# Performance work log

Hardware: AMD Instinct MI355X
Metric: run time of the kernel (lower is better)

## Reference

```python
import jax, jax.numpy as jnp
import numpy as np

BN_EPS = 1e-3  # O-CNN default bn_eps


def setup_inputs() -> dict:
    key = jax.random.key(0)
    k1, k2, k3 = jax.random.split(key, 3)
    N, Cin, Cout, K = 100000, 32, 32, 27  # nodes, channels, 3x3x3 taps
    data_in = jax.random.normal(k1, (1, Cin, N, 1), dtype=jnp.float32)
    neigh = jax.random.randint(k2, (N, K), 0, N, dtype=jnp.int32)
    weight = jax.random.normal(k3, (K, Cin, Cout), dtype=jnp.float32) * 0.05
    gamma = jnp.ones((Cout,), dtype=jnp.float32)
    beta = jnp.zeros((Cout,), dtype=jnp.float32)
    return {"data_in": data_in, "neigh": neigh, "weight": weight,
            "gamma": gamma, "beta": beta}


def reference(data_in, neigh, weight, gamma, beta):
    # data_in: [1, Cin, N, 1] -> x: [N, Cin]
    x = data_in[0, :, :, 0].T
    # Octree conv: gather 27 neighbor features per node, then small matmul.
    col = x[neigh]                                   # [N, 27, Cin] (irregular gather)
    y = jnp.einsum('nkc,kcd->nd', col, weight)       # [N, Cout]
    # BatchNorm2d in training mode: stats over the N (spatial) axis.
    mean = jnp.mean(y, axis=0)
    var = jnp.mean(jnp.square(y - mean), axis=0)     # biased variance, as BN uses
    yn = (y - mean) * jax.lax.rsqrt(var + BN_EPS) * gamma + beta
    # back to O-CNN layout [1, Cout, N, 1]
    return yn.T[None, :, :, None]
```

## Files before the change

### kernel.cpp

```cpp
#include <hip/hip_runtime.h>

#define KK 27

typedef short bf16x8 __attribute__((ext_vector_type(8)));
typedef float f32x4  __attribute__((ext_vector_type(4)));

__device__ inline unsigned short f2bf(float f) {
    unsigned u = __float_as_uint(f);
    unsigned r = u + 0x7fffu + ((u >> 16) & 1u);
    return (unsigned short)(r >> 16);
}

__global__ __launch_bounds__(256) void prep_k(const float* __restrict__ in,
                                              const float* __restrict__ w,
                                              unsigned short* __restrict__ xTb,
                                              unsigned short* __restrict__ wTb,
                                              float* __restrict__ tot,
                                              int N, int nxblk) {
    __shared__ float tile[32][33];
    const int b = blockIdx.x;
    if (b < nxblk) {
        int n0 = b * 32;
        int tx = threadIdx.x & 31;
        int ty = threadIdx.x >> 5;
#pragma unroll
        for (int c = ty; c < 32; c += 8) {
            int n = n0 + tx;
            tile[c][tx] = (n < N) ? in[(long)c * N + n] : 0.f;
        }
        __syncthreads();
#pragma unroll
        for (int nn = ty; nn < 32; nn += 8) {
            int n = n0 + nn;
            if (n < N) xTb[(long)n * 32 + tx] = f2bf(tile[tx][nn]);
        }
        if (b == 0 && threadIdx.x < 32) xTb[(long)N * 32 + threadIdx.x] = 0;
    } else {
        int k = b - nxblk;
        for (int i = threadIdx.x; i < 1024; i += 256) {
            int cin = i >> 5, cout = i & 31;
            wTb[k * 1024 + cout * 32 + cin] = f2bf(w[k * 1024 + cin * 32 + cout]);
        }
        if (k == 0) {
            for (int i = threadIdx.x; i < 32 * 64; i += 256) tot[i] = 0.f;
        }
    }
}

__global__ __launch_bounds__(64, 4) void conv_k(const unsigned short* __restrict__ xTb,
                                                const int* __restrict__ neigh,
                                                const unsigned short* __restrict__ wTb,
                                                float* __restrict__ y,
                                                float* __restrict__ tot,
                                                int N) {
    __shared__ float ct[16][33];

    const int L    = threadIdx.x;
    const int r16  = L & 15;
    const int quad = L >> 4;
    const int base = blockIdx.x * 16;
    const int n0   = base + r16;
    const bool v0  = (n0 < N);
    const long nb0 = (long)(v0 ? n0 : 0) * KK;

    f32x4 acc0 = {0.f, 0.f, 0.f, 0.f};
    f32x4 acc1 = acc0;

    bf16x8 A[3], B0[3], B1[3];
    int ja[3];

#pragma unroll
    for (int d = 0; d < 3; ++d) ja[d] = v0 ? neigh[nb0 + d] : N;
#pragma unroll
    for (int d = 0; d < 3; ++d) {
        A[d]  = *(const bf16x8*)(xTb + (long)ja[d] * 32 + quad * 8);
        const unsigned short* wn = wTb + d * 1024;
        B0[d] = *(const bf16x8*)(wn + r16 * 32 + quad * 8);
        B1[d] = *(const bf16x8*)(wn + (16 + r16) * 32 + quad * 8);
        ja[d] = v0 ? neigh[nb0 + d + 3] : N;
    }

#pragma unroll
    for (int t = 0; t < KK; ++t) {
        const int cur = t % 3;
        acc0 = __builtin_amdgcn_mfma_f32_16x16x32_bf16(A[cur], B0[cur], acc0, 0, 0, 0);
        acc1 = __builtin_amdgcn_mfma_f32_16x16x32_bf16(A[cur], B1[cur], acc1, 0, 0, 0);
        if (t + 3 < KK) {
            A[cur]  = *(const bf16x8*)(xTb + (long)ja[cur] * 32 + quad * 8);
            const unsigned short* wn = wTb + (t + 3) * 1024;
            B0[cur] = *(const bf16x8*)(wn + r16 * 32 + quad * 8);
            B1[cur] = *(const bf16x8*)(wn + (16 + r16) * 32 + quad * 8);
            if (t + 6 < KK) ja[cur] = v0 ? neigh[nb0 + t + 6] : N;
        }
    }

    float s0 = 0.f, q0 = 0.f, s1 = 0.f, q1 = 0.f;
#pragma unroll
    for (int r = 0; r < 4; ++r) {
        s0 += acc0[r];
        q0 += acc0[r] * acc0[r];
        s1 += acc1[r];
        q1 += acc1[r] * acc1[r];
    }
#pragma unroll
    for (int off = 16; off < 64; off <<= 1) {
        s0 += __shfl_xor(s0, off, 64);
        q0 += __shfl_xor(q0, off, 64);
        s1 += __shfl_xor(s1, off, 64);
        q1 += __shfl_xor(q1, off, 64);
    }
    const int stripe = blockIdx.x & 31;
    if (L < 16) {
        float* tb = tot + stripe * 64;
        atomicAdd(&tb[L],      s0);
        atomicAdd(&tb[L + 16], s1);
        atomicAdd(&tb[L + 32], q0);
        atomicAdd(&tb[L + 48], q1);
    }

#pragma unroll
    for (int r = 0; r < 4; ++r) {
        ct[quad * 4 + r][r16]      = acc0[r];
        ct[quad * 4 + r][16 + r16] = acc1[r];
    }
    __syncthreads();
    const int node = L & 15;
    const int ch   = L >> 4;
    const int gn   = base + node;
    if (gn < N) {
#pragma unroll
        for (int i = 0; i < 8; ++i) {
            const int cout = ch * 8 + i;
            y[(long)cout * N + gn] = ct[node][cout];
        }
    }
}

__global__ __launch_bounds__(256) void norm_k(float* __restrict__ y,
                                              const float* __restrict__ tot,
                                              const float* __restrict__ gamma,
                                              const float* __restrict__ beta, int N) {
    const int d = blockIdx.y;
    float sm = 0.f, sq = 0.f;
#pragma unroll
    for (int s = 0; s < 32; ++s) {
        sm += tot[s * 64 + d];
        sq += tot[s * 64 + 32 + d];
    }
    const float mean = sm / (float)N;
    const float var  = sq / (float)N - mean * mean;
    const float sc   = gamma[d] * rsqrtf(var + 1e-3f);
    const float sh   = beta[d] - mean * sc;

    int i = blockIdx.x * blockDim.x + threadIdx.x;
    int base = i * 4;
    if (base + 3 < N) {
        float4* p = (float4*)(y + (long)d * N + base);
        float4 v = *p;
        v.x = fmaf(v.x, sc, sh);
        v.y = fmaf(v.y, sc, sh);
        v.z = fmaf(v.z, sc, sh);
        v.w = fmaf(v.w, sc, sh);
        *p = v;
    } else if (base < N) {
        for (int t = base; t < N; ++t) y[(long)d * N + t] = fmaf(y[(long)d * N + t], sc, sh);
    }
}

extern "C" void kernel_launch(void* const* d_in, const int* in_sizes, int n_in,
                              void* d_out, int out_size, void* d_ws, size_t ws_size,
                              hipStream_t stream) {
    const float* data_in = (const float*)d_in[0];
    const int*   neigh   = (const int*)d_in[1];
    const float* weight  = (const float*)d_in[2];
    const float* gamma   = (const float*)d_in[3];
    const float* beta    = (const float*)d_in[4];
    float* out = (float*)d_out;

    const int N = in_sizes[1] / KK;
    const int nxblk  = (N + 31) / 32;
    const int nblk16 = (N + 15) / 16;

    char* ws = (char*)d_ws;
    unsigned short* xTb = (unsigned short*)ws;
    unsigned short* wTb = (unsigned short*)(ws + (size_t)(N + 1) * 64);
    float* tot = (float*)(ws + (size_t)(N + 1) * 64 + 55296);

    prep_k<<<nxblk + KK, 256, 0, stream>>>(data_in, weight, xTb, wTb, tot, N, nxblk);
    conv_k<<<nblk16, 64, 0, stream>>>(xTb, neigh, wTb, out, tot, N);
    dim3 ngrid(((N + 3) / 4 + 255) / 256, 32);
    norm_k<<<ngrid, 256, 0, stream>>>(out, tot, gamma, beta, N);
}
```

Measured before the change: 135.6 us.

## Process 32 nodes per wave in 256-thread conv blocks, sharing weight fragments

The conv kernel now uses 4-wave blocks, and each wave computes two 16-node MFMA tiles. The B weight fragments are loaded once per tap and reused for both node tiles. Output stores now cover 32 contiguous nodes per channel, and the block-wide barrier is dropped because each wave uses its own LDS slice. The three-deep register prefetch with full unrolling becomes a one-deep prefetch in a non-unrolled loop, which may leave more gather latency exposed.

```diff
diff --git a/kernel.cpp b/kernel.cpp
--- a/kernel.cpp
+++ b/kernel.cpp
@@ -47,60 +47,73 @@
     }
 }
 
-__global__ __launch_bounds__(64, 4) void conv_k(const unsigned short* __restrict__ xTb,
-                                                const int* __restrict__ neigh,
-                                                const unsigned short* __restrict__ wTb,
-                                                float* __restrict__ y,
-                                                float* __restrict__ tot,
-                                                int N) {
-    __shared__ float ct[16][33];
-
-    const int L    = threadIdx.x;
+__global__ __launch_bounds__(256, 4) void conv_k(const unsigned short* __restrict__ xTb,
+                                                 const int* __restrict__ neigh,
+                                                 const unsigned short* __restrict__ wTb,
+                                                 float* __restrict__ y,
+                                                 float* __restrict__ tot,
+                                                 int N) {
+    __shared__ float ct[4][32][33];
+
+    const int tid  = threadIdx.x;
+    const int L    = tid & 63;
+    const int w    = tid >> 6;
     const int r16  = L & 15;
     const int quad = L >> 4;
-    const int base = blockIdx.x * 16;
-    const int n0   = base + r16;
-    const bool v0  = (n0 < N);
+    const int base = blockIdx.x * 128 + w * 32;
+    const int n0 = base + r16;
+    const int n1 = base + 16 + r16;
+    const bool v0 = (n0 < N), v1 = (n1 < N);
     const long nb0 = (long)(v0 ? n0 : 0) * KK;
-
-    f32x4 acc0 = {0.f, 0.f, 0.f, 0.f};
-    f32x4 acc1 = acc0;
-
-    bf16x8 A[3], B0[3], B1[3];
-    int ja[3];
-
-#pragma unroll
-    for (int d = 0; d < 3; ++d) ja[d] = v0 ? neigh[nb0 + d] : N;
-#pragma unroll
-    for (int d = 0; d < 3; ++d) {
-        A[d]  = *(const bf16x8*)(xTb + (long)ja[d] * 32 + quad * 8);
-        const unsigned short* wn = wTb + d * 1024;
-        B0[d] = *(const bf16x8*)(wn + r16 * 32 + quad * 8);
-        B1[d] = *(const bf16x8*)(wn + (16 + r16) * 32 + quad * 8);
-        ja[d] = v0 ? neigh[nb0 + d + 3] : N;
-    }
-
-#pragma unroll
-    for (int t = 0; t < KK; ++t) {
-        const int cur = t % 3;
-        acc0 = __builtin_amdgcn_mfma_f32_16x16x32_bf16(A[cur], B0[cur], acc0, 0, 0, 0);
-        acc1 = __builtin_amdgcn_mfma_f32_16x16x32_bf16(A[cur], B1[cur], acc1, 0, 0, 0);
-        if (t + 3 < KK) {
-            A[cur]  = *(const bf16x8*)(xTb + (long)ja[cur] * 32 + quad * 8);
-            const unsigned short* wn = wTb + (t + 3) * 1024;
-            B0[cur] = *(const bf16x8*)(wn + r16 * 32 + quad * 8);
-            B1[cur] = *(const bf16x8*)(wn + (16 + r16) * 32 + quad * 8);
-            if (t + 6 < KK) ja[cur] = v0 ? neigh[nb0 + t + 6] : N;
+    const long nb1 = (long)(v1 ? n1 : 0) * KK;
+
+    f32x4 acc00 = {0.f, 0.f, 0.f, 0.f};
+    f32x4 acc01 = acc00, acc10 = acc00, acc11 = acc00;
+
+    int ia = v0 ? neigh[nb0] : N;
+    int ib = v1 ? neigh[nb1] : N;
+    int ja = v0 ? neigh[nb0 + 1] : N;
+    int jb = v1 ? neigh[nb1 + 1] : N;
+
+    bf16x8 a0 = *(const bf16x8*)(xTb + (long)ia * 32 + quad * 8);
+    bf16x8 a1 = *(const bf16x8*)(xTb + (long)ib * 32 + quad * 8);
+    bf16x8 b0 = *(const bf16x8*)(wTb + r16 * 32 + quad * 8);
+    bf16x8 b1 = *(const bf16x8*)(wTb + (16 + r16) * 32 + quad * 8);
+
+#pragma unroll 1
+    for (int k = 0; k < KK; ++k) {
+        bf16x8 na0, na1, pb0, pb1;
+        if (k < KK - 1) {
+            na0 = *(const bf16x8*)(xTb + (long)ja * 32 + quad * 8);
+            na1 = *(const bf16x8*)(xTb + (long)jb * 32 + quad * 8);
+            const unsigned short* wn = wTb + (k + 1) * 1024;
+            pb0 = *(const bf16x8*)(wn + r16 * 32 + quad * 8);
+            pb1 = *(const bf16x8*)(wn + (16 + r16) * 32 + quad * 8);
+            int kk = (k + 2 < KK) ? (k + 2) : (KK - 1);
+            ja = v0 ? neigh[nb0 + kk] : N;
+            jb = v1 ? neigh[nb1 + kk] : N;
+        }
+
+        acc00 = __builtin_amdgcn_mfma_f32_16x16x32_bf16(a0, b0, acc00, 0, 0, 0);
+        acc01 = __builtin_amdgcn_mfma_f32_16x16x32_bf16(a0, b1, acc01, 0, 0, 0);
+        acc10 = __builtin_amdgcn_mfma_f32_16x16x32_bf16(a1, b0, acc10, 0, 0, 0);
+        acc11 = __builtin_amdgcn_mfma_f32_16x16x32_bf16(a1, b1, acc11, 0, 0, 0);
+
+        if (k < KK - 1) {
+            a0 = na0;
+            a1 = na1;
+            b0 = pb0;
+            b1 = pb1;
         }
     }
 
     float s0 = 0.f, q0 = 0.f, s1 = 0.f, q1 = 0.f;
 #pragma unroll
     for (int r = 0; r < 4; ++r) {
-        s0 += acc0[r];
-        q0 += acc0[r] * acc0[r];
-        s1 += acc1[r];
-        q1 += acc1[r] * acc1[r];
+        s0 += acc00[r] + acc10[r];
+        q0 += acc00[r] * acc00[r] + acc10[r] * acc10[r];
+        s1 += acc01[r] + acc11[r];
+        q1 += acc01[r] * acc01[r] + acc11[r] * acc11[r];
     }
 #pragma unroll
     for (int off = 16; off < 64; off <<= 1) {
@@ -109,7 +122,7 @@
         s1 += __shfl_xor(s1, off, 64);
         q1 += __shfl_xor(q1, off, 64);
     }
-    const int stripe = blockIdx.x & 31;
+    const int stripe = (blockIdx.x * 4 + w) & 31;
     if (L < 16) {
         float* tb = tot + stripe * 64;
         atomicAdd(&tb[L],      s0);
@@ -120,18 +133,19 @@
 
 #pragma unroll
     for (int r = 0; r < 4; ++r) {
-        ct[quad * 4 + r][r16]      = acc0[r];
-        ct[quad * 4 + r][16 + r16] = acc1[r];
-    }
-    __syncthreads();
-    const int node = L & 15;
-    const int ch   = L >> 4;
-    const int gn   = base + node;
+        ct[w][quad * 4 + r][r16]           = acc00[r];
+        ct[w][quad * 4 + r][16 + r16]      = acc01[r];
+        ct[w][16 + quad * 4 + r][r16]      = acc10[r];
+        ct[w][16 + quad * 4 + r][16 + r16] = acc11[r];
+    }
+    const int node = L & 31;
+    const int half = L >> 5;
+    const int gn = base + node;
     if (gn < N) {
 #pragma unroll
-        for (int i = 0; i < 8; ++i) {
-            const int cout = ch * 8 + i;
-            y[(long)cout * N + gn] = ct[node][cout];
+        for (int i = 0; i < 16; ++i) {
+            const int cout = i * 2 + half;
+            y[(long)cout * N + gn] = ct[w][node][cout];
         }
     }
 }
@@ -178,8 +192,8 @@
     float* out = (float*)d_out;
 
     const int N = in_sizes[1] / KK;
-    const int nxblk  = (N + 31) / 32;
-    const int nblk16 = (N + 15) / 16;
+    const int nxblk   = (N + 31) / 32;
+    const int nblk128 = (N + 127) / 128;
 
     char* ws = (char*)d_ws;
     unsigned short* xTb = (unsigned short*)ws;
@@ -187,7 +201,7 @@
     float* tot = (float*)(ws + (size_t)(N + 1) * 64 + 55296);
 
     prep_k<<<nxblk + KK, 256, 0, stream>>>(data_in, weight, xTb, wTb, tot, N, nxblk);
-    conv_k<<<nblk16, 64, 0, stream>>>(xTb, neigh, wTb, out, tot, N);
+    conv_k<<<nblk128, 256, 0, stream>>>(xTb, neigh, wTb, out, tot, N);
     dim3 ngrid(((N + 3) / 4 + 255) / 256, 32);
     norm_k<<<ngrid, 256, 0, stream>>>(out, tot, gamma, beta, N);
 }
```

Measured after the change: 146.8 us. 1.08x slower.
